# Kernel optimization log

Measured on AMD Instinct MI355X. Metric: run time of the kernel, lower is better.

Reference implementation:

```python
import jax, jax.numpy as jnp
from jax import lax
import numpy as np

B, TIN, F, H, TOUT = 256, 512, 64, 512, 64


def setup_inputs() -> dict:
    key = jax.random.key(0)
    ks = jax.random.split(key, 16)
    s = 0.05

    def p(k, shape):
        return jax.random.normal(k, shape, jnp.float32) * s

    inp = {
        "x": jax.random.normal(ks[0], (B, TIN, F), jnp.float32),
        "y": jax.random.normal(ks[1], (B, TOUT), jnp.float32),
    }
    i = 2
    for name, insz in [("enc0", F), ("enc1", H), ("dec0", 1), ("dec1", H)]:
        inp[name + "_Wih"] = p(ks[i], (4 * H, insz)); i += 1
        inp[name + "_Whh"] = p(ks[i], (4 * H, H)); i += 1
        inp[name + "_bih"] = jnp.zeros((4 * H,), jnp.float32)
        inp[name + "_bhh"] = jnp.zeros((4 * H,), jnp.float32)
    inp["proj_W"] = p(ks[i], (1, H)); i += 1
    inp["proj_b"] = jnp.zeros((1,), jnp.float32)
    return inp


def _cell(xt, h, c, Wih, Whh, bih, bhh):
    # PyTorch gate order: i, f, g, o
    g = xt @ Wih.T + h @ Whh.T + bih + bhh  # [B, 4H]
    i, f, gg, o = jnp.split(g, 4, axis=-1)
    c = jax.nn.sigmoid(f) * c + jax.nn.sigmoid(i) * jnp.tanh(gg)
    h = jax.nn.sigmoid(o) * jnp.tanh(c)
    return h, c


def reference(x, y,
              enc0_Wih, enc0_Whh, enc0_bih, enc0_bhh,
              enc1_Wih, enc1_Whh, enc1_bih, enc1_bhh,
              dec0_Wih, dec0_Whh, dec0_bih, dec0_bhh,
              dec1_Wih, dec1_Whh, dec1_bih, dec1_bhh,
              proj_W, proj_b):
    Bsz = x.shape[0]
    Hd = enc0_Whh.shape[1]
    Tout = y.shape[1]
    z = jnp.zeros((Bsz, Hd), x.dtype)

    def enc_step(carry, xt):
        h0, c0, h1, c1 = carry
        h0, c0 = _cell(xt, h0, c0, enc0_Wih, enc0_Whh, enc0_bih, enc0_bhh)
        h1, c1 = _cell(h0, h1, c1, enc1_Wih, enc1_Whh, enc1_bih, enc1_bhh)
        return (h0, c0, h1, c1), None

    (h0, c0, h1, c1), _ = lax.scan(enc_step, (z, z, z, z), jnp.swapaxes(x, 0, 1))

    prev = x[:, -1, -1:]  # [B, 1]

    def dec_step(carry, _):
        h0, c0, h1, c1, prev = carry
        h0, c0 = _cell(prev, h0, c0, dec0_Wih, dec0_Whh, dec0_bih, dec0_bhh)
        h1, c1 = _cell(h0, h1, c1, dec1_Wih, dec1_Whh, dec1_bih, dec1_bhh)
        step = h1 @ proj_W.T + proj_b  # [B, 1]
        # teacher_forcing = 0.0 -> always feed model prediction back
        return (h0, c0, h1, c1, step), step[:, 0]

    _, outs = lax.scan(dec_step, (h0, c0, h1, c1, prev), None, length=Tout)
    return outs.T  # [B, Tout]
```

## Files before the change

### kernel.cpp

```cpp
#include <hip/hip_runtime.h>

#define TINN 512
#define FF 64
#define HHD 512
#define TOUTN 64

using v8h = __attribute__((ext_vector_type(8))) _Float16;
using v4h = __attribute__((ext_vector_type(4))) _Float16;
using v4f = __attribute__((ext_vector_type(4))) float;
using u32x4 = __attribute__((ext_vector_type(4))) unsigned int;
using u64 = unsigned long long;

#define AGT __HIP_MEMORY_SCOPE_AGENT

#define WOFF 0
#define BIAS_OFF 131072
#define WIH0_OFF 131328
#define PREV_OFF 131584
#define PART_OFF 131840
#define PROJW_OFF 132864
#define PROJB_OFF 134912
#define TRANS_OFF 134976
#define SMEM_TOTAL 137024

#define WS_BAR 0
#define WS_FLAG_BYTES (4 * 64 * 64 * 64)
#define WS_HOFF WS_FLAG_BYTES
#define HBYTES (256 * HHD * 2)
#define WS_XS (WS_HOFF + 6 * HBYTES)
#define XS_TBYTES 32768
#define WS_NEED (WS_XS + (size_t)TINN * XS_TBYTES)

static __device__ __forceinline__ float sigm(float x) { return 1.0f / (1.0f + __expf(-x)); }
static __device__ __forceinline__ float tanh_f(float x) { return 1.0f - 2.0f / (1.0f + __expf(2.0f * x)); }

static __device__ __forceinline__ v8h aload16(const _Float16* p) {
  union { u64 u[2]; v8h h; } c;
  const u64* q = (const u64*)p;
  c.u[0] = __hip_atomic_load(q, __ATOMIC_RELAXED, AGT);
  c.u[1] = __hip_atomic_load(q + 1, __ATOMIC_RELAXED, AGT);
  return c.h;
}
static __device__ __forceinline__ void astore8(_Float16* p, v4h v) {
  union { u64 u; v4h h; } c;
  c.h = v;
  __hip_atomic_store((u64*)p, c.u, __ATOMIC_RELAXED, AGT);
}
static __device__ __forceinline__ void astore8z(void* p) {
  __hip_atomic_store((u64*)p, 0ull, __ATOMIC_RELAXED, AGT);
}

#if __has_builtin(__builtin_amdgcn_raw_ptr_buffer_load_b128) && \
    __has_builtin(__builtin_amdgcn_make_buffer_rsrc)
#define HAVE_BUFLOAD 1
using rsrc_t = __amdgpu_buffer_rsrc_t;
static __device__ __forceinline__ rsrc_t mkrsrc(const void* p) {
  return __builtin_amdgcn_make_buffer_rsrc((void*)p, (short)0, 0xFFFFFFFFu, 0x00020000);
}
static __device__ __forceinline__ v8h bload16(rsrc_t r, int byteOff) {
  union { u32x4 u; v8h h; } c;
  c.u = __builtin_amdgcn_raw_ptr_buffer_load_b128(r, byteOff, 0, 17);
  return c.h;
}
#endif

static __device__ __forceinline__ void signalDone(unsigned* flagsG, int mySlot, unsigned val) {
  __builtin_amdgcn_s_waitcnt(0);
  __syncthreads();
  if (threadIdx.x < 64) {
    unsigned* p = flagsG + ((size_t)threadIdx.x * 64 + mySlot) * 16;
    __hip_atomic_store(p, val, __ATOMIC_RELAXED, AGT);
  }
}

static __device__ __forceinline__ void waitRolePriv(unsigned* myflags, int base, int tgt) {
  if (tgt > 0) {
    if (threadIdx.x < 32) {
      unsigned* p = myflags + (size_t)(base + threadIdx.x) * 16;
      while ((int)__hip_atomic_load(p, __ATOMIC_RELAXED, AGT) < tgt)
        __builtin_amdgcn_s_sleep(1);
    }
    __syncthreads();
#if __has_builtin(__builtin_amdgcn_sched_barrier)
    __builtin_amdgcn_sched_barrier(0);
#endif
  }
}

static __device__ __forceinline__ void waitRolesPriv(unsigned* myflags, int tgt0, int tgt1) {
  int t = threadIdx.x;
  if (t < 64) {
    int tgt = (t < 32) ? tgt0 : tgt1;
    if (tgt > 0) {
      unsigned* p = myflags + (size_t)t * 16;
      while ((int)__hip_atomic_load(p, __ATOMIC_RELAXED, AGT) < tgt)
        __builtin_amdgcn_s_sleep(1);
    }
  }
  __syncthreads();
#if __has_builtin(__builtin_amdgcn_sched_barrier)
  __builtin_amdgcn_sched_barrier(0);
#endif
}

static __device__ __attribute__((noinline)) void loadWeights(
    int tid, int hc0, const float* W1, int ld1, int K1,
    const float* W2, int K) {
  extern __shared__ char smem[];
  int c = tid >> 2, sub = tid & 3;
  int nt = c >> 4, l = c & 15;
  int n = nt * HHD + hc0 + l;
  int Kq = K >> 2;
  for (int k = sub * Kq; k < (sub + 1) * Kq; ++k) {
    float v;
    if (k < K1) v = W1[(size_t)n * ld1 + k];
    else        v = W2[(size_t)n * HHD + (k - K1)];
    int kc = k >> 6, ks = (k >> 5) & 1, quad = (k >> 3) & 3, j = k & 7;
    int off = (((kc * 2 + ks) * 4 + nt) * 64 + quad * 16 + l) * 16 + j * 2;
    *(_Float16*)(smem + WOFF + off) = (_Float16)v;
  }
}

template <int WC0>
static __device__ __forceinline__ void mfma8(
    const _Float16* src, int rt, int lane, const char* wbLane, v4f* acc) {
#if HAVE_BUFLOAD
  rsrc_t rs = mkrsrc(src);
#endif
#pragma unroll
  for (int kc = 0; kc < 8; ++kc) {
    int off = rt * 16384 + kc * 2048 + lane * 16;
    v8h ak0, ak1;
#if HAVE_BUFLOAD
    ak0 = bload16(rs, off);
    ak1 = bload16(rs, off + 1024);
#else
    ak0 = aload16(src + off / 2);
    ak1 = aload16(src + (off + 1024) / 2);
#endif
    const char* bb = wbLane + (size_t)(WC0 + kc) * 8192;
#pragma unroll
    for (int ks = 0; ks < 2; ++ks) {
      v8h a = ks ? ak1 : ak0;
      acc[0] = __builtin_amdgcn_mfma_f32_16x16x32_f16(a, *(const v8h*)(bb + (ks * 4 + 0) * 1024), acc[0], 0, 0, 0);
      acc[1] = __builtin_amdgcn_mfma_f32_16x16x32_f16(a, *(const v8h*)(bb + (ks * 4 + 1) * 1024), acc[1], 0, 0, 0);
      acc[2] = __builtin_amdgcn_mfma_f32_16x16x32_f16(a, *(const v8h*)(bb + (ks * 4 + 2) * 1024), acc[2], 0, 0, 0);
      acc[3] = __builtin_amdgcn_mfma_f32_16x16x32_f16(a, *(const v8h*)(bb + (ks * 4 + 3) * 1024), acc[3], 0, 0, 0);
    }
  }
}

static __device__ __forceinline__ void mfmaDual(
    const _Float16* h0src, const _Float16* h1src, int rt, int lane,
    const char* wbLane, v4f* acc) {
  v8h a1[16], a0[16];
#if HAVE_BUFLOAD
  rsrc_t r1 = mkrsrc(h1src);
  rsrc_t r0 = mkrsrc(h0src);
#pragma unroll
  for (int kc = 0; kc < 8; ++kc) {
    int off = rt * 16384 + kc * 2048 + lane * 16;
    a1[2 * kc]     = bload16(r1, off);
    a1[2 * kc + 1] = bload16(r1, off + 1024);
  }
#pragma unroll
  for (int kc = 0; kc < 8; ++kc) {
    int off = rt * 16384 + kc * 2048 + lane * 16;
    a0[2 * kc]     = bload16(r0, off);
    a0[2 * kc + 1] = bload16(r0, off + 1024);
  }
#else
#pragma unroll
  for (int kc = 0; kc < 8; ++kc) {
    int off = rt * 16384 + kc * 2048 + lane * 16;
    a1[2 * kc]     = aload16(h1src + off / 2);
    a1[2 * kc + 1] = aload16(h1src + (off + 1024) / 2);
  }
#pragma unroll
  for (int kc = 0; kc < 8; ++kc) {
    int off = rt * 16384 + kc * 2048 + lane * 16;
    a0[2 * kc]     = aload16(h0src + off / 2);
    a0[2 * kc + 1] = aload16(h0src + (off + 1024) / 2);
  }
#endif
#pragma unroll
  for (int kc = 0; kc < 8; ++kc) {
    const char* bb = wbLane + (size_t)(8 + kc) * 8192;
#pragma unroll
    for (int ks = 0; ks < 2; ++ks) {
      v8h a = a1[2 * kc + ks];
      acc[0] = __builtin_amdgcn_mfma_f32_16x16x32_f16(a, *(const v8h*)(bb + (ks * 4 + 0) * 1024), acc[0], 0, 0, 0);
      acc[1] = __builtin_amdgcn_mfma_f32_16x16x32_f16(a, *(const v8h*)(bb + (ks * 4 + 1) * 1024), acc[1], 0, 0, 0);
      acc[2] = __builtin_amdgcn_mfma_f32_16x16x32_f16(a, *(const v8h*)(bb + (ks * 4 + 2) * 1024), acc[2], 0, 0, 0);
      acc[3] = __builtin_amdgcn_mfma_f32_16x16x32_f16(a, *(const v8h*)(bb + (ks * 4 + 3) * 1024), acc[3], 0, 0, 0);
    }
  }
#pragma unroll
  for (int kc = 0; kc < 8; ++kc) {
    const char* bb = wbLane + (size_t)kc * 8192;
#pragma unroll
    for (int ks = 0; ks < 2; ++ks) {
      v8h a = a0[2 * kc + ks];
      acc[0] = __builtin_amdgcn_mfma_f32_16x16x32_f16(a, *(const v8h*)(bb + (ks * 4 + 0) * 1024), acc[0], 0, 0, 0);
      acc[1] = __builtin_amdgcn_mfma_f32_16x16x32_f16(a, *(const v8h*)(bb + (ks * 4 + 1) * 1024), acc[1], 0, 0, 0);
      acc[2] = __builtin_amdgcn_mfma_f32_16x16x32_f16(a, *(const v8h*)(bb + (ks * 4 + 2) * 1024), acc[2], 0, 0, 0);
      acc[3] = __builtin_amdgcn_mfma_f32_16x16x32_f16(a, *(const v8h*)(bb + (ks * 4 + 3) * 1024), acc[3], 0, 0, 0);
    }
  }
}

static __device__ __forceinline__ void xChunk(
    const char* xsT, const float* xstep, int m0, int tid,
    const char* wbLane, v4f* acc) {
  int lane = tid & 63, wave = tid >> 6;
  int l15 = lane & 15, quad = lane >> 4;
  v8h ak0, ak1;
  if (xsT != nullptr) {
    int rt = (m0 >> 4) + wave;
    const char* xb = xsT + rt * 2048 + lane * 16;
    ak0 = *(const v8h*)(xb);
    ak1 = *(const v8h*)(xb + 1024);
  } else {
    int ra = m0 + wave * 16 + l15;
    const float* xr = xstep + (size_t)ra * (TINN * FF) + quad * 8;
    v4f f00 = *(const v4f*)(xr);
    v4f f01 = *(const v4f*)(xr + 4);
    v4f f10 = *(const v4f*)(xr + 32);
    v4f f11 = *(const v4f*)(xr + 36);
#pragma unroll
    for (int e = 0; e < 4; ++e) {
      ak0[e] = (_Float16)f00[e]; ak0[4 + e] = (_Float16)f01[e];
      ak1[e] = (_Float16)f10[e]; ak1[4 + e] = (_Float16)f11[e];
    }
  }
#pragma unroll
  for (int ks = 0; ks < 2; ++ks) {
    v8h a = ks ? ak1 : ak0;
    acc[0] = __builtin_amdgcn_mfma_f32_16x16x32_f16(a, *(const v8h*)(wbLane + (ks * 4 + 0) * 1024), acc[0], 0, 0, 0);
    acc[1] = __builtin_amdgcn_mfma_f32_16x16x32_f16(a, *(const v8h*)(wbLane + (ks * 4 + 1) * 1024), acc[1], 0, 0, 0);
    acc[2] = __builtin_amdgcn_mfma_f32_16x16x32_f16(a, *(const v8h*)(wbLane + (ks * 4 + 2) * 1024), acc[2], 0, 0, 0);
    acc[3] = __builtin_amdgcn_mfma_f32_16x16x32_f16(a, *(const v8h*)(wbLane + (ks * 4 + 3) * 1024), acc[3], 0, 0, 0);
  }
}

static __device__ __forceinline__ void epilogue(
    int tid, int m0, int hc0, int rank1, _Float16* hout, float* creg, v4f* acc) {
  extern __shared__ char smem[];
  int lane = tid & 63, wave = tid >> 6;
  int l15 = lane & 15, quad = lane >> 4;
  float* bias = (float*)(smem + BIAS_OFF);
  float bi = bias[l15], bf = bias[16 + l15], bg = bias[32 + l15], bo = bias[48 + l15];
  float wi = 0.f, wf = 0.f, wg = 0.f, wo = 0.f;
  if (rank1) {
    float* wih0 = (float*)(smem + WIH0_OFF);
    wi = wih0[l15]; wf = wih0[16 + l15]; wg = wih0[32 + l15]; wo = wih0[48 + l15];
  }
  float* prevl = (float*)(smem + PREV_OFF);
  _Float16* tb = (_Float16*)(smem + TRANS_OFF + (size_t)wave * 512);
#pragma unroll
  for (int r = 0; r < 4; ++r) {
    int mloc = wave * 16 + quad * 4 + r;
    float gi = acc[0][r] + bi, gf = acc[1][r] + bf;
    float gg = acc[2][r] + bg, go = acc[3][r] + bo;
    if (rank1) {
      float pv = prevl[mloc];
      gi += pv * wi; gf += pv * wf; gg += pv * wg; go += pv * wo;
    }
    float cc = sigm(gf) * creg[r] + sigm(gi) * tanh_f(gg);
    float h = sigm(go) * tanh_f(cc);
    creg[r] = cc;
    tb[(quad * 4 + r) * 16 + l15] = (_Float16)h;
  }
  {
    int mloc = lane & 15, cg = lane >> 4;
    v4h hv = *(const v4h*)(tb + mloc * 16 + cg * 4);
    int m = m0 + wave * 16 + mloc;
    int c0 = hc0 + cg * 4;
    int off = (m >> 4) * 16384 + (c0 >> 6) * 2048 + ((c0 >> 5) & 1) * 1024 +
              ((c0 >> 3) & 3) * 256 + (m & 15) * 16 + (c0 & 7) * 2;
    astore8((_Float16*)((char*)hout + off), hv);
  }
}


static __device__ __attribute__((noinline)) void stepEnc0(
    int tid, int m0, int hc0, unsigned* flagsG, unsigned* myflags, int mySlot, int p,
    const char* xsT, const float* xstep,
    const _Float16* h0prev, _Float16* h0out, float* creg) {
  extern __shared__ char smem[];
  int lane = tid & 63, wave = tid >> 6;
  v4f acc[4];
  acc[0] = v4f{0.f, 0.f, 0.f, 0.f}; acc[1] = acc[0]; acc[2] = acc[0]; acc[3] = acc[0];
  const char* wbLane = smem + WOFF + (size_t)lane * 16;
  if (p == 0) {
    waitRolesPriv(myflags, 1, 0);
    xChunk(xsT, xstep, m0, tid, wbLane, acc);
  } else {
    xChunk(xsT, xstep, m0, tid, wbLane, acc);
    waitRolesPriv(myflags, p + 1, p - 2);
  }
  mfma8<1>(h0prev, (m0 >> 4) + wave, lane, wbLane, acc);
  epilogue(tid, m0, hc0, 0, h0out, creg, acc);
  signalDone(flagsG, mySlot, p + 2);
}

static __device__ __attribute__((noinline)) void stepL1(
    int tid, int m0, int hc0, unsigned* flagsG, unsigned* myflags, int mySlot,
    int tR1, int tR0,
    const _Float16* h0src, const _Float16* h1prev, _Float16* h1out, float* creg) {
  extern __shared__ char smem[];
  int lane = tid & 63, wave = tid >> 6;
  v4f acc[4];
  acc[0] = v4f{0.f, 0.f, 0.f, 0.f}; acc[1] = acc[0]; acc[2] = acc[0]; acc[3] = acc[0];
  const char* wbLane = smem + WOFF + (size_t)lane * 16;
  int rt = (m0 >> 4) + wave;
  waitRolesPriv(myflags, tR0, tR1);
  mfmaDual(h0src, h1prev, rt, lane, wbLane, acc);
  epilogue(tid, m0, hc0, 0, h1out, creg, acc);
  signalDone(flagsG, mySlot, tR0);
}

static __device__ __attribute__((noinline)) void stepDec0(
    int tid, int m0, int hc0, unsigned* flagsG, unsigned* myflags, int mySlot, int u,
    const _Float16* h0prev, _Float16* h0out, float* creg) {
  extern __shared__ char smem[];
  int lane = tid & 63, wave = tid >> 6;
  v4f acc[4];
  acc[0] = v4f{0.f, 0.f, 0.f, 0.f}; acc[1] = acc[0]; acc[2] = acc[0]; acc[3] = acc[0];
  const char* wbLane = smem + WOFF + (size_t)lane * 16;
  waitRolePriv(myflags, 0, u + 1);
  mfma8<0>(h0prev, (m0 >> 4) + wave, lane, wbLane, acc);
  epilogue(tid, m0, hc0, 1, h0out, creg, acc);
  signalDone(flagsG, mySlot, u + 2);
}

__global__ void __launch_bounds__(256, 1)
seq2seq_kernel(const float* x,
               const float* e0wi, const float* e0wh, const float* e0bi, const float* e0bh,
               const float* e1wi, const float* e1wh, const float* e1bi, const float* e1bh,
               const float* d0wi, const float* d0wh, const float* d0bi, const float* d0bh,
               const float* d1wi, const float* d1wh, const float* d1bi, const float* d1bh,
               const float* pw, const float* pb,
               float* out, char* ws, int useXs) {
  extern __shared__ char smem[];
  int tid = threadIdx.x, bid = blockIdx.x;
  int group = bid >> 6;
  int r = bid & 63;
  bool isL1 = (r >= 32);
  int hcTile = r & 31;
  int hc0 = hcTile * 16;
  int m0 = group * 64;
  unsigned* flagsG = (unsigned*)(ws + WS_BAR) + (size_t)group * 64 * 64 * 16;
  unsigned* myflags = flagsG + (size_t)r * 64 * 16;
  int mySlot = isL1 ? 32 + hcTile : hcTile;
  char* xs = useXs ? (ws + WS_XS) : nullptr;

  _Float16* h0b[4]; _Float16* h1b[2];
  h0b[0] = (_Float16*)(ws + WS_HOFF);
  h0b[1] = (_Float16*)(ws + WS_HOFF + 1 * HBYTES);
  h0b[2] = (_Float16*)(ws + WS_HOFF + 2 * HBYTES);
  h0b[3] = (_Float16*)(ws + WS_HOFF + 3 * HBYTES);
  h1b[0] = (_Float16*)(ws + WS_HOFF + 4 * HBYTES);
  h1b[1] = (_Float16*)(ws + WS_HOFF + 5 * HBYTES);

  float creg[4];
  creg[0] = 0.f; creg[1] = 0.f; creg[2] = 0.f; creg[3] = 0.f;

  {
    int t16 = r * 256 + tid;
    char* base = (t16 < 8192) ? (char*)h0b[3] : (char*)h1b[1];
    int idx = t16 & 8191;
    astore8z(base + (size_t)m0 * HHD * 2 + (size_t)idx * 8);
  }

  if (xs) {
    int m = m0 + (tid & 63);
    int cb = (tid >> 6) * 16;
    int rt = m >> 4, l15m = m & 15;
    for (int k = 0; k < 8; ++k) {
      int t = r + k * 64;
      const float* xp = x + (size_t)m * (TINN * FF) + (size_t)t * FF + cb;
      v4f f0 = *(const v4f*)(xp);
      v4f f1 = *(const v4f*)(xp + 4);
      v4f f2 = *(const v4f*)(xp + 8);
      v4f f3 = *(const v4f*)(xp + 12);
      v4h h0_, h1_, h2_, h3_;
#pragma unroll
      for (int e = 0; e < 4; ++e) {
        h0_[e] = (_Float16)f0[e]; h1_[e] = (_Float16)f1[e];
        h2_[e] = (_Float16)f2[e]; h3_[e] = (_Float16)f3[e];
      }
      char* xt = xs + (size_t)t * XS_TBYTES;
      v4h hs[4] = {h0_, h1_, h2_, h3_};
#pragma unroll
      for (int s = 0; s < 4; ++s) {
        int c0 = cb + 4 * s;
        int off = (rt * 2 + ((c0 >> 5) & 1)) * 1024 +
                  ((c0 >> 3) & 3) * 256 + l15m * 16 + (c0 & 7) * 2;
        astore8((_Float16*)(xt + off), hs[s]);
      }
    }
  }

  if (!isL1) {
    loadWeights(tid, hc0, e0wi, 64, 64, e0wh, 576);
    if (tid < 64) {
      int n = (tid >> 4) * HHD + hc0 + (tid & 15);
      ((float*)(smem + BIAS_OFF))[tid] = e0bi[n] + e0bh[n];
    }
  } else {
    loadWeights(tid, hc0, e1wi, 512, 512, e1wh, 1024);
    if (tid < 64) {
      int n = (tid >> 4) * HHD + hc0 + (tid & 15);
      ((float*)(smem + BIAS_OFF))[tid] = e1bi[n] + e1bh[n];
    }
  }
  signalDone(flagsG, mySlot, 1);

  if (!isL1) {
    for (int p = 0; p < TINN; ++p)
      stepEnc0(tid, m0, hc0, flagsG, myflags, mySlot, p,
               xs ? xs + (size_t)p * XS_TBYTES : nullptr,
               xs ? nullptr : x + (size_t)p * FF,
               h0b[(p + 3) & 3], h0b[p & 3], creg);
    loadWeights(tid, hc0, d0wh, 512, 512, nullptr, 512);
    if (tid < 64) {
      int n = (tid >> 4) * HHD + hc0 + (tid & 15);
      ((float*)(smem + BIAS_OFF))[tid] = d0bi[n] + d0bh[n];
      ((float*)(smem + WIH0_OFF))[tid] = d0wi[n];
    }
    for (int k = tid; k < 512; k += 256) ((float*)(smem + PROJW_OFF))[k] = pw[k];
    if (tid == 0) ((float*)(smem + PROJB_OFF))[0] = pb[0];
    for (int t = 0; t <= TOUTN; ++t) {
      int u = TINN + t;
      waitRolePriv(myflags, 32, u + 1);
      float* prevl = (float*)(smem + PREV_OFF);
      if (t == 0) {
        if (tid < 64)
          prevl[tid] = x[(size_t)(m0 + tid) * (TINN * FF) + 511 * 64 + 63];
      } else {
        float* part = (float*)(smem + PART_OFF);
        float* pjw = (float*)(smem + PROJW_OFF);
        const _Float16* h1base = h1b[(u + 1) & 1];
        int m = m0 + (tid >> 2);
        int rt = m >> 4, l15m = m & 15;
        int kc0 = (tid & 3) * 2;
        float s = 0.f;
#pragma unroll
        for (int kc = kc0; kc < kc0 + 2; ++kc)
#pragma unroll
          for (int ks = 0; ks < 2; ++ks)
#pragma unroll
            for (int q = 0; q < 4; ++q) {
              int off = (rt * 8 + kc) * 2048 + ks * 1024 + q * 256 + l15m * 16;
              v8h hv = aload16(h1base + off / 2);
              const float* w = pjw + kc * 64 + ks * 32 + q * 8;
#pragma unroll
              for (int e = 0; e < 8; ++e) s += (float)hv[e] * w[e];
            }
        part[tid] = s;
        __syncthreads();
        if (tid < 64) {
          float p4 = part[tid * 4] + part[tid * 4 + 1] + part[tid * 4 + 2] +
                     part[tid * 4 + 3] + ((float*)(smem + PROJB_OFF))[0];
          prevl[tid] = p4;
          if (hcTile == 0) out[(size_t)(m0 + tid) * TOUTN + (t - 1)] = p4;
        }
      }
      __syncthreads();
      if (t < TOUTN)
        stepDec0(tid, m0, hc0, flagsG, myflags, mySlot, u,
                 h0b[(u + 3) & 3], h0b[u & 3], creg);
    }
  } else {
    for (int s = 0; s < TINN; ++s)
      stepL1(tid, m0, hc0, flagsG, myflags, mySlot, s + 1, s + 2,
             h0b[s & 3], h1b[(s + 1) & 1], h1b[s & 1], creg);
    loadWeights(tid, hc0, d1wi, 512, 512, d1wh, 1024);
    if (tid < 64) {
      int n = (tid >> 4) * HHD + hc0 + (tid & 15);
      ((float*)(smem + BIAS_OFF))[tid] = d1bi[n] + d1bh[n];
    }
    for (int t = 0; t < TOUTN; ++t) {
      int u = TINN + t;
      stepL1(tid, m0, hc0, flagsG, myflags, mySlot, u + 1, u + 2,
             h0b[u & 3], h1b[(u + 1) & 1], h1b[u & 1], creg);
    }
  }
}

extern "C" void kernel_launch(void* const* d_in, const int* in_sizes, int n_in,
                              void* d_out, int out_size, void* d_ws, size_t ws_size,
                              hipStream_t stream) {
  const float* x = (const float*)d_in[0];
  const float* e0wi = (const float*)d_in[2];
  const float* e0wh = (const float*)d_in[3];
  const float* e0bi = (const float*)d_in[4];
  const float* e0bh = (const float*)d_in[5];
  const float* e1wi = (const float*)d_in[6];
  const float* e1wh = (const float*)d_in[7];
  const float* e1bi = (const float*)d_in[8];
  const float* e1bh = (const float*)d_in[9];
  const float* d0wi = (const float*)d_in[10];
  const float* d0wh = (const float*)d_in[11];
  const float* d0bi = (const float*)d_in[12];
  const float* d0bh = (const float*)d_in[13];
  const float* d1wi = (const float*)d_in[14];
  const float* d1wh = (const float*)d_in[15];
  const float* d1bi = (const float*)d_in[16];
  const float* d1bh = (const float*)d_in[17];
  const float* pw = (const float*)d_in[18];
  const float* pb = (const float*)d_in[19];

  int useXs = (ws_size >= WS_NEED) ? 1 : 0;
  (void)hipFuncSetAttribute((const void*)seq2seq_kernel,
                            hipFuncAttributeMaxDynamicSharedMemorySize, SMEM_TOTAL);
  (void)hipMemsetAsync(d_ws, 0, WS_FLAG_BYTES, stream);
  seq2seq_kernel<<<dim3(256), dim3(256), SMEM_TOTAL, stream>>>(
      x, e0wi, e0wh, e0bi, e0bh, e1wi, e1wh, e1bi, e1bh,
      d0wi, d0wh, d0bi, d0bh, d1wi, d1wh, d1bi, d1bh,
      pw, pb, (float*)d_out, (char*)d_ws, useXs);
}
```

Baseline: 4.453 ms.

## Deepen hidden-state ring buffers and use cached loads with periodic acquire fences

Replaces the 4-deep/2-deep hidden-state buffers with 32-deep rings when the workspace is large enough. The state is then read with plain cached vector loads instead of per-load coherent atomic or buffer loads, and an agent-scope acquire fence runs only every 24 steps to invalidate stale cache lines. The fp16 x-staging pre-pass is dropped, so x is converted inline every step. This relies on ring depth to keep stale cached data from being read between fences, which is a subtle memory-ordering correctness risk.

Result: slower. 4.564 ms (+2.5%).

```diff
diff --git a/kernel.cpp b/kernel.cpp
--- a/kernel.cpp
+++ b/kernel.cpp
@@ -27,9 +27,8 @@
 #define WS_FLAG_BYTES (4 * 64 * 64 * 64)
 #define WS_HOFF WS_FLAG_BYTES
 #define HBYTES (256 * HHD * 2)
-#define WS_XS (WS_HOFF + 6 * HBYTES)
-#define XS_TBYTES 32768
-#define WS_NEED (WS_XS + (size_t)TINN * XS_TBYTES)
+#define WS_NEED_DEEP (WS_FLAG_BYTES + (size_t)64 * HBYTES)
+#define INV_PERIOD 24
 
 static __device__ __forceinline__ float sigm(float x) { return 1.0f / (1.0f + __expf(-x)); }
 static __device__ __forceinline__ float tanh_f(float x) { return 1.0f - 2.0f / (1.0f + __expf(2.0f * x)); }
@@ -48,6 +47,9 @@
 }
 static __device__ __forceinline__ void astore8z(void* p) {
   __hip_atomic_store((u64*)p, 0ull, __ATOMIC_RELAXED, AGT);
+}
+static __device__ __forceinline__ void acquireFence() {
+  __builtin_amdgcn_fence(__ATOMIC_ACQUIRE, "agent");
 }
 
 #if __has_builtin(__builtin_amdgcn_raw_ptr_buffer_load_b128) && \
@@ -121,23 +123,29 @@
   }
 }
 
-template <int WC0>
+template <int WC0, bool DEEP>
 static __device__ __forceinline__ void mfma8(
     const _Float16* src, int rt, int lane, const char* wbLane, v4f* acc) {
 #if HAVE_BUFLOAD
-  rsrc_t rs = mkrsrc(src);
+  rsrc_t rs;
+  if constexpr (!DEEP) rs = mkrsrc(src);
 #endif
 #pragma unroll
   for (int kc = 0; kc < 8; ++kc) {
     int off = rt * 16384 + kc * 2048 + lane * 16;
     v8h ak0, ak1;
+    if constexpr (DEEP) {
+      ak0 = *(const v8h*)((const char*)src + off);
+      ak1 = *(const v8h*)((const char*)src + off + 1024);
+    } else {
 #if HAVE_BUFLOAD
-    ak0 = bload16(rs, off);
-    ak1 = bload16(rs, off + 1024);
+      ak0 = bload16(rs, off);
+      ak1 = bload16(rs, off + 1024);
 #else
-    ak0 = aload16(src + off / 2);
-    ak1 = aload16(src + (off + 1024) / 2);
+      ak0 = aload16(src + off / 2);
+      ak1 = aload16(src + (off + 1024) / 2);
 #endif
+    }
     const char* bb = wbLane + (size_t)(WC0 + kc) * 8192;
 #pragma unroll
     for (int ks = 0; ks < 2; ++ks) {
@@ -150,39 +158,55 @@
   }
 }
 
+template <bool DEEP>
 static __device__ __forceinline__ void mfmaDual(
     const _Float16* h0src, const _Float16* h1src, int rt, int lane,
     const char* wbLane, v4f* acc) {
   v8h a1[16], a0[16];
+  if constexpr (DEEP) {
+#pragma unroll
+    for (int kc = 0; kc < 8; ++kc) {
+      int off = rt * 16384 + kc * 2048 + lane * 16;
+      a1[2 * kc]     = *(const v8h*)((const char*)h1src + off);
+      a1[2 * kc + 1] = *(const v8h*)((const char*)h1src + off + 1024);
+    }
+#pragma unroll
+    for (int kc = 0; kc < 8; ++kc) {
+      int off = rt * 16384 + kc * 2048 + lane * 16;
+      a0[2 * kc]     = *(const v8h*)((const char*)h0src + off);
+      a0[2 * kc + 1] = *(const v8h*)((const char*)h0src + off + 1024);
+    }
+  } else {
 #if HAVE_BUFLOAD
-  rsrc_t r1 = mkrsrc(h1src);
-  rsrc_t r0 = mkrsrc(h0src);
-#pragma unroll
-  for (int kc = 0; kc < 8; ++kc) {
-    int off = rt * 16384 + kc * 2048 + lane * 16;
-    a1[2 * kc]     = bload16(r1, off);
-    a1[2 * kc + 1] = bload16(r1, off + 1024);
-  }
-#pragma unroll
-  for (int kc = 0; kc < 8; ++kc) {
-    int off = rt * 16384 + kc * 2048 + lane * 16;
-    a0[2 * kc]     = bload16(r0, off);
-    a0[2 * kc + 1] = bload16(r0, off + 1024);
-  }
+    rsrc_t r1 = mkrsrc(h1src);
+    rsrc_t r0 = mkrsrc(h0src);
+#pragma unroll
+    for (int kc = 0; kc < 8; ++kc) {
+      int off = rt * 16384 + kc * 2048 + lane * 16;
+      a1[2 * kc]     = bload16(r1, off);
+      a1[2 * kc + 1] = bload16(r1, off + 1024);
+    }
+#pragma unroll
+    for (int kc = 0; kc < 8; ++kc) {
+      int off = rt * 16384 + kc * 2048 + lane * 16;
+      a0[2 * kc]     = bload16(r0, off);
+      a0[2 * kc + 1] = bload16(r0, off + 1024);
+    }
 #else
 #pragma unroll
-  for (int kc = 0; kc < 8; ++kc) {
-    int off = rt * 16384 + kc * 2048 + lane * 16;
-    a1[2 * kc]     = aload16(h1src + off / 2);
-    a1[2 * kc + 1] = aload16(h1src + (off + 1024) / 2);
-  }
-#pragma unroll
-  for (int kc = 0; kc < 8; ++kc) {
-    int off = rt * 16384 + kc * 2048 + lane * 16;
-    a0[2 * kc]     = aload16(h0src + off / 2);
-    a0[2 * kc + 1] = aload16(h0src + (off + 1024) / 2);
-  }
+    for (int kc = 0; kc < 8; ++kc) {
+      int off = rt * 16384 + kc * 2048 + lane * 16;
+      a1[2 * kc]     = aload16(h1src + off / 2);
+      a1[2 * kc + 1] = aload16(h1src + (off + 1024) / 2);
+    }
+#pragma unroll
+    for (int kc = 0; kc < 8; ++kc) {
+      int off = rt * 16384 + kc * 2048 + lane * 16;
+      a0[2 * kc]     = aload16(h0src + off / 2);
+      a0[2 * kc + 1] = aload16(h0src + (off + 1024) / 2);
+    }
 #endif
+  }
 #pragma unroll
   for (int kc = 0; kc < 8; ++kc) {
     const char* bb = wbLane + (size_t)(8 + kc) * 8192;
@@ -210,28 +234,20 @@
 }
 
 static __device__ __forceinline__ void xChunk(
-    const char* xsT, const float* xstep, int m0, int tid,
-    const char* wbLane, v4f* acc) {
+    const float* xstep, int m0, int tid, const char* wbLane, v4f* acc) {
   int lane = tid & 63, wave = tid >> 6;
   int l15 = lane & 15, quad = lane >> 4;
   v8h ak0, ak1;
-  if (xsT != nullptr) {
-    int rt = (m0 >> 4) + wave;
-    const char* xb = xsT + rt * 2048 + lane * 16;
-    ak0 = *(const v8h*)(xb);
-    ak1 = *(const v8h*)(xb + 1024);
-  } else {
-    int ra = m0 + wave * 16 + l15;
-    const float* xr = xstep + (size_t)ra * (TINN * FF) + quad * 8;
-    v4f f00 = *(const v4f*)(xr);
-    v4f f01 = *(const v4f*)(xr + 4);
-    v4f f10 = *(const v4f*)(xr + 32);
-    v4f f11 = *(const v4f*)(xr + 36);
-#pragma unroll
-    for (int e = 0; e < 4; ++e) {
-      ak0[e] = (_Float16)f00[e]; ak0[4 + e] = (_Float16)f01[e];
-      ak1[e] = (_Float16)f10[e]; ak1[4 + e] = (_Float16)f11[e];
-    }
+  int ra = m0 + wave * 16 + l15;
+  const float* xr = xstep + (size_t)ra * (TINN * FF) + quad * 8;
+  v4f f00 = *(const v4f*)(xr);
+  v4f f01 = *(const v4f*)(xr + 4);
+  v4f f10 = *(const v4f*)(xr + 32);
+  v4f f11 = *(const v4f*)(xr + 36);
+#pragma unroll
+  for (int e = 0; e < 4; ++e) {
+    ak0[e] = (_Float16)f00[e]; ak0[4 + e] = (_Float16)f01[e];
+    ak1[e] = (_Float16)f10[e]; ak1[4 + e] = (_Float16)f11[e];
   }
 #pragma unroll
   for (int ks = 0; ks < 2; ++ks) {
@@ -283,31 +299,30 @@
 }
 
 
+template <bool DEEP>
 static __device__ __attribute__((noinline)) void stepEnc0(
     int tid, int m0, int hc0, unsigned* flagsG, unsigned* myflags, int mySlot, int p,
-    const char* xsT, const float* xstep,
-    const _Float16* h0prev, _Float16* h0out, float* creg) {
+    const float* xstep, const _Float16* h0prev, _Float16* h0out, float* creg,
+    bool doInv) {
   extern __shared__ char smem[];
   int lane = tid & 63, wave = tid >> 6;
   v4f acc[4];
   acc[0] = v4f{0.f, 0.f, 0.f, 0.f}; acc[1] = acc[0]; acc[2] = acc[0]; acc[3] = acc[0];
   const char* wbLane = smem + WOFF + (size_t)lane * 16;
-  if (p == 0) {
-    waitRolesPriv(myflags, 1, 0);
-    xChunk(xsT, xstep, m0, tid, wbLane, acc);
-  } else {
-    xChunk(xsT, xstep, m0, tid, wbLane, acc);
-    waitRolesPriv(myflags, p + 1, p - 2);
-  }
-  mfma8<1>(h0prev, (m0 >> 4) + wave, lane, wbLane, acc);
+  xChunk(xstep, m0, tid, wbLane, acc);
+  waitRolesPriv(myflags, p + 1, p - 2);
+  if (DEEP && doInv) acquireFence();
+  mfma8<1, DEEP>(h0prev, (m0 >> 4) + wave, lane, wbLane, acc);
   epilogue(tid, m0, hc0, 0, h0out, creg, acc);
   signalDone(flagsG, mySlot, p + 2);
 }
 
+template <bool DEEP>
 static __device__ __attribute__((noinline)) void stepL1(
     int tid, int m0, int hc0, unsigned* flagsG, unsigned* myflags, int mySlot,
     int tR1, int tR0,
-    const _Float16* h0src, const _Float16* h1prev, _Float16* h1out, float* creg) {
+    const _Float16* h0src, const _Float16* h1prev, _Float16* h1out, float* creg,
+    bool doInv) {
   extern __shared__ char smem[];
   int lane = tid & 63, wave = tid >> 6;
   v4f acc[4];
@@ -315,25 +330,29 @@
   const char* wbLane = smem + WOFF + (size_t)lane * 16;
   int rt = (m0 >> 4) + wave;
   waitRolesPriv(myflags, tR0, tR1);
-  mfmaDual(h0src, h1prev, rt, lane, wbLane, acc);
+  if (DEEP && doInv) acquireFence();
+  mfmaDual<DEEP>(h0src, h1prev, rt, lane, wbLane, acc);
   epilogue(tid, m0, hc0, 0, h1out, creg, acc);
   signalDone(flagsG, mySlot, tR0);
 }
 
+template <bool DEEP>
 static __device__ __attribute__((noinline)) void stepDec0(
     int tid, int m0, int hc0, unsigned* flagsG, unsigned* myflags, int mySlot, int u,
-    const _Float16* h0prev, _Float16* h0out, float* creg) {
+    const _Float16* h0prev, _Float16* h0out, float* creg, bool doInv) {
   extern __shared__ char smem[];
   int lane = tid & 63, wave = tid >> 6;
   v4f acc[4];
   acc[0] = v4f{0.f, 0.f, 0.f, 0.f}; acc[1] = acc[0]; acc[2] = acc[0]; acc[3] = acc[0];
   const char* wbLane = smem + WOFF + (size_t)lane * 16;
   waitRolePriv(myflags, 0, u + 1);
-  mfma8<0>(h0prev, (m0 >> 4) + wave, lane, wbLane, acc);
+  if (DEEP && doInv) acquireFence();
+  mfma8<0, DEEP>(h0prev, (m0 >> 4) + wave, lane, wbLane, acc);
   epilogue(tid, m0, hc0, 1, h0out, creg, acc);
   signalDone(flagsG, mySlot, u + 2);
 }
 
+template <bool DEEP>
 __global__ void __launch_bounds__(256, 1)
 seq2seq_kernel(const float* x,
                const float* e0wi, const float* e0wh, const float* e0bi, const float* e0bh,
@@ -341,8 +360,10 @@
                const float* d0wi, const float* d0wh, const float* d0bi, const float* d0bh,
                const float* d1wi, const float* d1wh, const float* d1bi, const float* d1bh,
                const float* pw, const float* pb,
-               float* out, char* ws, int useXs) {
+               float* out, char* ws) {
   extern __shared__ char smem[];
+  constexpr int D0M = DEEP ? 31 : 3;
+  constexpr int D1M = DEEP ? 31 : 1;
   int tid = threadIdx.x, bid = blockIdx.x;
   int group = bid >> 6;
   int r = bid & 63;
@@ -353,53 +374,19 @@
   unsigned* flagsG = (unsigned*)(ws + WS_BAR) + (size_t)group * 64 * 64 * 16;
   unsigned* myflags = flagsG + (size_t)r * 64 * 16;
   int mySlot = isL1 ? 32 + hcTile : hcTile;
-  char* xs = useXs ? (ws + WS_XS) : nullptr;
-
-  _Float16* h0b[4]; _Float16* h1b[2];
-  h0b[0] = (_Float16*)(ws + WS_HOFF);
-  h0b[1] = (_Float16*)(ws + WS_HOFF + 1 * HBYTES);
-  h0b[2] = (_Float16*)(ws + WS_HOFF + 2 * HBYTES);
-  h0b[3] = (_Float16*)(ws + WS_HOFF + 3 * HBYTES);
-  h1b[0] = (_Float16*)(ws + WS_HOFF + 4 * HBYTES);
-  h1b[1] = (_Float16*)(ws + WS_HOFF + 5 * HBYTES);
+
+  char* h0ring = ws + WS_HOFF;
+  char* h1ring = ws + WS_HOFF + (size_t)(D0M + 1) * HBYTES;
 
   float creg[4];
   creg[0] = 0.f; creg[1] = 0.f; creg[2] = 0.f; creg[3] = 0.f;
 
   {
     int t16 = r * 256 + tid;
-    char* base = (t16 < 8192) ? (char*)h0b[3] : (char*)h1b[1];
+    char* base = (t16 < 8192) ? (h0ring + (size_t)D0M * HBYTES)
+                              : (h1ring + (size_t)D1M * HBYTES);
     int idx = t16 & 8191;
     astore8z(base + (size_t)m0 * HHD * 2 + (size_t)idx * 8);
-  }
-
-  if (xs) {
-    int m = m0 + (tid & 63);
-    int cb = (tid >> 6) * 16;
-    int rt = m >> 4, l15m = m & 15;
-    for (int k = 0; k < 8; ++k) {
-      int t = r + k * 64;
-      const float* xp = x + (size_t)m * (TINN * FF) + (size_t)t * FF + cb;
-      v4f f0 = *(const v4f*)(xp);
-      v4f f1 = *(const v4f*)(xp + 4);
-      v4f f2 = *(const v4f*)(xp + 8);
-      v4f f3 = *(const v4f*)(xp + 12);
-      v4h h0_, h1_, h2_, h3_;
-#pragma unroll
-      for (int e = 0; e < 4; ++e) {
-        h0_[e] = (_Float16)f0[e]; h1_[e] = (_Float16)f1[e];
-        h2_[e] = (_Float16)f2[e]; h3_[e] = (_Float16)f3[e];
-      }
-      char* xt = xs + (size_t)t * XS_TBYTES;
-      v4h hs[4] = {h0_, h1_, h2_, h3_};
-#pragma unroll
-      for (int s = 0; s < 4; ++s) {
-        int c0 = cb + 4 * s;
-        int off = (rt * 2 + ((c0 >> 5) & 1)) * 1024 +
-                  ((c0 >> 3) & 3) * 256 + l15m * 16 + (c0 & 7) * 2;
-        astore8((_Float16*)(xt + off), hs[s]);
-      }
-    }
   }
 
   if (!isL1) {
@@ -419,10 +406,11 @@
 
   if (!isL1) {
     for (int p = 0; p < TINN; ++p)
-      stepEnc0(tid, m0, hc0, flagsG, myflags, mySlot, p,
-               xs ? xs + (size_t)p * XS_TBYTES : nullptr,
-               xs ? nullptr : x + (size_t)p * FF,
-               h0b[(p + 3) & 3], h0b[p & 3], creg);
+      stepEnc0<DEEP>(tid, m0, hc0, flagsG, myflags, mySlot, p,
+                     x + (size_t)p * FF,
+                     (const _Float16*)(h0ring + (size_t)((p + D0M) & D0M) * HBYTES),
+                     (_Float16*)(h0ring + (size_t)(p & D0M) * HBYTES),
+                     creg, (p % INV_PERIOD) == 0);
     loadWeights(tid, hc0, d0wh, 512, 512, nullptr, 512);
     if (tid < 64) {
       int n = (tid >> 4) * HHD + hc0 + (tid & 15);
@@ -441,7 +429,8 @@
       } else {
         float* part = (float*)(smem + PART_OFF);
         float* pjw = (float*)(smem + PROJW_OFF);
-        const _Float16* h1base = h1b[(u + 1) & 1];
+        const _Float16* h1base =
+            (const _Float16*)(h1ring + (size_t)((u + D1M) & D1M) * HBYTES);
         int m = m0 + (tid >> 2);
         int rt = m >> 4, l15m = m & 15;
         int kc0 = (tid & 3) * 2;
@@ -469,13 +458,18 @@
       }
       __syncthreads();
       if (t < TOUTN)
-        stepDec0(tid, m0, hc0, flagsG, myflags, mySlot, u,
-                 h0b[(u + 3) & 3], h0b[u & 3], creg);
+        stepDec0<DEEP>(tid, m0, hc0, flagsG, myflags, mySlot, u,
+                       (const _Float16*)(h0ring + (size_t)((u + D0M) & D0M) * HBYTES),
+                       (_Float16*)(h0ring + (size_t)(u & D0M) * HBYTES),
+                       creg, (u % INV_PERIOD) == 0);
     }
   } else {
     for (int s = 0; s < TINN; ++s)
-      stepL1(tid, m0, hc0, flagsG, myflags, mySlot, s + 1, s + 2,
-             h0b[s & 3], h1b[(s + 1) & 1], h1b[s & 1], creg);
+      stepL1<DEEP>(tid, m0, hc0, flagsG, myflags, mySlot, s + 1, s + 2,
+                   (const _Float16*)(h0ring + (size_t)(s & D0M) * HBYTES),
+                   (const _Float16*)(h1ring + (size_t)((s + D1M) & D1M) * HBYTES),
+                   (_Float16*)(h1ring + (size_t)(s & D1M) * HBYTES),
+                   creg, (s % INV_PERIOD) == 0);
     loadWeights(tid, hc0, d1wi, 512, 512, d1wh, 1024);
     if (tid < 64) {
       int n = (tid >> 4) * HHD + hc0 + (tid & 15);
@@ -483,8 +477,11 @@
     }
     for (int t = 0; t < TOUTN; ++t) {
       int u = TINN + t;
-      stepL1(tid, m0, hc0, flagsG, myflags, mySlot, u + 1, u + 2,
-             h0b[u & 3], h1b[(u + 1) & 1], h1b[u & 1], creg);
+      stepL1<DEEP>(tid, m0, hc0, flagsG, myflags, mySlot, u + 1, u + 2,
+                   (const _Float16*)(h0ring + (size_t)(u & D0M) * HBYTES),
+                   (const _Float16*)(h1ring + (size_t)((u + D1M) & D1M) * HBYTES),
+                   (_Float16*)(h1ring + (size_t)(u & D1M) * HBYTES),
+                   creg, (u % INV_PERIOD) == 0);
     }
   }
 }
@@ -512,12 +509,21 @@
   const float* pw = (const float*)d_in[18];
   const float* pb = (const float*)d_in[19];
 
-  int useXs = (ws_size >= WS_NEED) ? 1 : 0;
-  (void)hipFuncSetAttribute((const void*)seq2seq_kernel,
-                            hipFuncAttributeMaxDynamicSharedMemorySize, SMEM_TOTAL);
+  bool deep = (ws_size >= WS_NEED_DEEP);
   (void)hipMemsetAsync(d_ws, 0, WS_FLAG_BYTES, stream);
-  seq2seq_kernel<<<dim3(256), dim3(256), SMEM_TOTAL, stream>>>(
-      x, e0wi, e0wh, e0bi, e0bh, e1wi, e1wh, e1bi, e1bh,
-      d0wi, d0wh, d0bi, d0bh, d1wi, d1wh, d1bi, d1bh,
-      pw, pb, (float*)d_out, (char*)d_ws, useXs);
-}
+  if (deep) {
+    (void)hipFuncSetAttribute((const void*)seq2seq_kernel<true>,
+                              hipFuncAttributeMaxDynamicSharedMemorySize, SMEM_TOTAL);
+    seq2seq_kernel<true><<<dim3(256), dim3(256), SMEM_TOTAL, stream>>>(
+        x, e0wi, e0wh, e0bi, e0bh, e1wi, e1wh, e1bi, e1bh,
+        d0wi, d0wh, d0bi, d0bh, d1wi, d1wh, d1bi, d1bh,
+        pw, pb, (float*)d_out, (char*)d_ws);
+  } else {
+    (void)hipFuncSetAttribute((const void*)seq2seq_kernel<false>,
+                              hipFuncAttributeMaxDynamicSharedMemorySize, SMEM_TOTAL);
+    seq2seq_kernel<false><<<dim3(256), dim3(256), SMEM_TOTAL, stream>>>(
+        x, e0wi, e0wh, e0bi, e0bh, e1wi, e1wh, e1bi, e1bh,
+        d0wi, d0wh, d0bi, d0bh, d1wi, d1wh, d1bi, d1bh,
+        pw, pb, (float*)d_out, (char*)d_ws);
+  }
+}
```
